# Kernel optimization log

Measured on AMD Instinct MI355X. Metric: run time of the kernel, lower is better.

Reference implementation:

```python
import jax, jax.numpy as jnp
import numpy as np
import math

L, B, T, E, HQ, HKV, V = 6, 4, 1024, 1024, 16, 4, 32000
D = E // HQ          # head dim = 64
G = HQ // HKV        # group size = 4
EKV = E // G         # kv proj dim = 256


def setup_inputs() -> dict:
    key = jax.random.key(0)
    ks = jax.random.split(key, 16)
    def n(k, shape):
        return jax.random.normal(k, shape, jnp.float32) * 0.02
    return dict(
        idx=jax.random.randint(ks[0], (B, T), 0, V),
        wte=n(ks[1], (V, E)),
        Wq=n(ks[2], (L, E, E)), bq=jnp.zeros((L, E), jnp.float32),
        Wk=n(ks[3], (L, EKV, E)), bk=jnp.zeros((L, EKV), jnp.float32),
        Wv=n(ks[4], (L, EKV, E)), bv=jnp.zeros((L, EKV), jnp.float32),
        Wo=n(ks[5], (L, E, E)), bo=jnp.zeros((L, E), jnp.float32),
        ln1_w=jnp.ones((L, E), jnp.float32), ln1_b=jnp.zeros((L, E), jnp.float32),
        ln2_w=jnp.ones((L, E), jnp.float32), ln2_b=jnp.zeros((L, E), jnp.float32),
        Wfc=n(ks[6], (L, 4 * E, E)), bfc=jnp.zeros((L, 4 * E), jnp.float32),
        Wproj=n(ks[7], (L, E, 4 * E)), bproj=jnp.zeros((L, E), jnp.float32),
        lnf_w=jnp.ones((E,), jnp.float32), lnf_b=jnp.zeros((E,), jnp.float32),
        lm_head=n(ks[8], (V, E)),
    )


def _ln(x, w, b):
    m = x.mean(-1, keepdims=True)
    v = ((x - m) ** 2).mean(-1, keepdims=True)
    return (x - m) * jax.lax.rsqrt(v + 1e-5) * w + b


def _gelu_new(x):
    c = math.sqrt(2.0 / math.pi)
    return 0.5 * x * (1.0 + jnp.tanh(c * (x + 0.044715 * x ** 3)))


def _rope_tables(t, d):
    # positions start at 1; thetas = base^(-2*(i-1)/d), i = 1..d/2
    pos = jnp.arange(1, t + 1, dtype=jnp.float32)
    thetas = 10000.0 ** (-2.0 * jnp.arange(d // 2, dtype=jnp.float32) / d)
    ang = pos[:, None] * thetas                      # [t, d/2]
    cos = jnp.concatenate([jnp.cos(ang)] * 2, -1)    # [t, d]
    sin = jnp.concatenate([jnp.sin(ang)] * 2, -1)
    return cos, sin


def _apply_rope(x, cos, sin):
    # x: [b, h, t, d]; x_cos = x; x_sin = concat(-right, left)
    x1, x2 = x[..., : D // 2], x[..., D // 2:]
    return x * cos + jnp.concatenate([-x2, x1], -1) * sin


def _gpt_forward(idx, wte, Wq, bq, Wk, bk, Wv, bv, Wo, bo,
                 ln1_w, ln1_b, ln2_w, ln2_b, Wfc, bfc, Wproj, bproj,
                 lnf_w, lnf_b, lm_head):
    cos, sin = _rope_tables(T, D)
    mask = jnp.tril(jnp.ones((T, T), bool))          # causal
    scale = 1.0 / math.sqrt(D)
    x = wte[idx]                                     # [B, T, E]
    for l in range(L):
        h = _ln(x, ln1_w[l], ln1_b[l])
        q = (h @ Wq[l].T + bq[l]).reshape(B, T, HQ, D).transpose(0, 2, 1, 3)
        k = (h @ Wk[l].T + bk[l]).reshape(B, T, HKV, D).transpose(0, 2, 1, 3)
        v = (h @ Wv[l].T + bv[l]).reshape(B, T, HKV, D).transpose(0, 2, 1, 3)
        q = _apply_rope(q, cos, sin)
        k = _apply_rope(k, cos, sin)
        q = q.reshape(B, HKV, G, T, D)               # kv-major head grouping
        att = jnp.einsum('bhgqd,bhkd->bhgqk', q, k) * scale
        att = jnp.where(mask, att, -jnp.inf)
        att = jax.nn.softmax(att, axis=-1)
        y = jnp.einsum('bhgqk,bhkd->bhgqd', att, v)
        y = y.transpose(0, 3, 1, 2, 4).reshape(B, T, E)   # b q (h g d)
        x = x + (y @ Wo[l].T + bo[l])
        h2 = _ln(x, ln2_w[l], ln2_b[l])
        ff = _gelu_new(h2 @ Wfc[l].T + bfc[l]) @ Wproj[l].T + bproj[l]
        x = x + ff
    x = _ln(x, lnf_w, lnf_b)
    return x @ lm_head.T                             # [B, T, V] logits


def reference(idx, wte, Wq, bq, Wk, bk, Wv, bv, Wo, bo,
              ln1_w, ln1_b, ln2_w, ln2_b, Wfc, bfc, Wproj, bproj,
              lnf_w, lnf_b, lm_head):
    return _gpt_forward(idx, wte, Wq, bq, Wk, bk, Wv, bv, Wo, bo,
                        ln1_w, ln1_b, ln2_w, ln2_b, Wfc, bfc, Wproj, bproj,
                        lnf_w, lnf_b, lm_head)
```

## Files before the change

### kernel.cpp

```cpp
#include <hip/hip_runtime.h>

#define Lz 6
#define Bz 4
#define Tz 1024
#define Ez 1024
#define HQz 16
#define HKVz 4
#define Dz 64
#define EKVz 256
#define Vz 32000
#define FFz 4096
#define QKVz 1536

typedef __attribute__((ext_vector_type(4))) float f32x4;
typedef __attribute__((ext_vector_type(8))) short short8;
typedef unsigned short ushort_t;

__device__ inline ushort_t f2b(float f) {
  union { float f; unsigned u; } x; x.f = f;
  unsigned r = x.u + 0x7fffu + ((x.u >> 16) & 1u);
  return (ushort_t)(r >> 16);
}
__device__ inline float b2f(ushort_t u) {
  union { unsigned u; float f; } x; x.u = ((unsigned)u) << 16;
  return x.f;
}
__device__ inline unsigned packbf(float lo, float hi) {
  return (unsigned)f2b(lo) | ((unsigned)f2b(hi) << 16);
}

__device__ inline void gload16(const void* g, void* l) {
  __builtin_amdgcn_global_load_lds(
      (const __attribute__((address_space(1))) void*)g,
      (__attribute__((address_space(3))) void*)l, 16, 0, 0);
}

template<int BIAS, int GELU, int WF32>
__global__ __launch_bounds__(512, 2) void gemm_bt256(
    const ushort_t* __restrict__ A, const ushort_t* __restrict__ Bw,
    const float* __restrict__ bias,
    float* __restrict__ Cf, ushort_t* __restrict__ Cb,
    int M, int N, int K)
{
  __shared__ ushort_t sA[2][2][128 * 64];
  __shared__ ushort_t sB[2][2][128 * 64];
  const int tid = threadIdx.x;
  const int lane = tid & 63, wid = tid >> 6;
  const int wr = wid >> 2, wc = wid & 3;
  const int l15 = lane & 15, l4 = lane >> 4;

  const int gx = gridDim.x;
  const int nwg = gx * gridDim.y;
  const int orig = blockIdx.y * gx + blockIdx.x;
  const int qq = nwg >> 3, rr = nwg & 7;
  const int xcd = orig & 7, loc = orig >> 3;
  const int swz = (xcd < rr) ? (xcd * (qq + 1) + loc)
                             : (rr * (qq + 1) + (xcd - rr) * qq + loc);
  const int bm = swz % gx, bn = swz / gx;

  const int NT = K >> 6;

  auto stage = [&](const ushort_t* src, int row_base, int k0, ushort_t* dst) {
#pragma unroll
    for (int i = 0; i < 2; ++i) {
      int s = i * 512 + tid;
      int row = s >> 3, jp = s & 7;
      int jlog = jp ^ (row & 7);
      gload16(src + (size_t)(row_base + row) * K + k0 + jlog * 8, (char*)dst + s * 16);
    }
  };

  stage(A,  bm * 256,       0, &sA[0][0][0]);
  stage(A,  bm * 256 + 128, 0, &sA[0][1][0]);
  stage(Bw, bn * 256,       0, &sB[0][0][0]);
  stage(Bw, bn * 256 + 128, 0, &sB[0][1][0]);
  stage(A,  bm * 256,       64, &sA[1][0][0]);
  stage(A,  bm * 256 + 128, 64, &sA[1][1][0]);
  stage(Bw, bn * 256,       64, &sB[1][0][0]);
  stage(Bw, bn * 256 + 128, 64, &sB[1][1][0]);
  asm volatile("s_waitcnt vmcnt(8)" ::: "memory");
  __builtin_amdgcn_sched_barrier(0);
  __builtin_amdgcn_s_barrier();
  __builtin_amdgcn_sched_barrier(0);

  f32x4 acc[8][4] = {};
  const int axc = l15 & 7;

  for (int t = 0; t < NT; ++t) {
    const int b = t & 1;
    const ushort_t* pA = &sA[b][wr][0];
    const ushort_t* pB = &sB[b][wc >> 1][(wc & 1) * 64 * 64];
    short8 aF[8][2], bF[4][2];

#pragma unroll
    for (int mt = 0; mt < 4; ++mt)
#pragma unroll
      for (int ks = 0; ks < 2; ++ks)
        aF[mt][ks] = *(const short8*)&pA[(mt * 16 + l15) * 64 + (((ks << 2) + l4) ^ axc) * 8];
#pragma unroll
    for (int nt = 0; nt < 4; ++nt)
      bF[nt][0] = *(const short8*)&pB[(nt * 16 + l15) * 64 + (l4 ^ axc) * 8];
    __builtin_amdgcn_s_setprio(1);
#pragma unroll
    for (int mt = 0; mt < 4; ++mt)
#pragma unroll
      for (int nt = 0; nt < 4; ++nt)
        acc[mt][nt] = __builtin_amdgcn_mfma_f32_16x16x32_bf16(aF[mt][0], bF[nt][0], acc[mt][nt], 0, 0, 0);
    __builtin_amdgcn_s_setprio(0);

#pragma unroll
    for (int mt = 4; mt < 8; ++mt)
#pragma unroll
      for (int ks = 0; ks < 2; ++ks)
        aF[mt][ks] = *(const short8*)&pA[(mt * 16 + l15) * 64 + (((ks << 2) + l4) ^ axc) * 8];
#pragma unroll
    for (int nt = 0; nt < 4; ++nt)
      bF[nt][1] = *(const short8*)&pB[(nt * 16 + l15) * 64 + ((4 + l4) ^ axc) * 8];
    __builtin_amdgcn_s_setprio(1);
#pragma unroll
    for (int mt = 0; mt < 4; ++mt)
#pragma unroll
      for (int nt = 0; nt < 4; ++nt)
        acc[mt][nt] = __builtin_amdgcn_mfma_f32_16x16x32_bf16(aF[mt][1], bF[nt][1], acc[mt][nt], 0, 0, 0);
    __builtin_amdgcn_s_setprio(0);

    asm volatile("s_waitcnt lgkmcnt(0)" ::: "memory");
    __builtin_amdgcn_sched_barrier(0);
    __builtin_amdgcn_s_barrier();
    __builtin_amdgcn_sched_barrier(0);

    const bool pf = (t + 2 < NT);
    if (pf) {
      const int k2 = (t + 2) << 6;
      stage(Bw, bn * 256,       k2, &sB[b][0][0]);
      stage(Bw, bn * 256 + 128, k2, &sB[b][1][0]);
    }
    __builtin_amdgcn_s_setprio(1);
#pragma unroll
    for (int mt = 4; mt < 8; ++mt)
#pragma unroll
      for (int nt = 0; nt < 4; ++nt)
        acc[mt][nt] = __builtin_amdgcn_mfma_f32_16x16x32_bf16(aF[mt][0], bF[nt][0], acc[mt][nt], 0, 0, 0);
    __builtin_amdgcn_s_setprio(0);

    if (pf) {
      const int k2 = (t + 2) << 6;
      stage(A, bm * 256,       k2, &sA[b][0][0]);
      stage(A, bm * 256 + 128, k2, &sA[b][1][0]);
    }
    __builtin_amdgcn_s_setprio(1);
#pragma unroll
    for (int mt = 4; mt < 8; ++mt)
#pragma unroll
      for (int nt = 0; nt < 4; ++nt)
        acc[mt][nt] = __builtin_amdgcn_mfma_f32_16x16x32_bf16(aF[mt][1], bF[nt][1], acc[mt][nt], 0, 0, 0);
    __builtin_amdgcn_s_setprio(0);

    if (t + 1 < NT) {
      if (pf) { asm volatile("s_waitcnt vmcnt(8)" ::: "memory"); }
      else    { asm volatile("s_waitcnt vmcnt(0)" ::: "memory"); }
      __builtin_amdgcn_sched_barrier(0);
      __builtin_amdgcn_s_barrier();
      __builtin_amdgcn_sched_barrier(0);
    }
  }

#pragma unroll
  for (int mt = 0; mt < 8; ++mt) {
#pragma unroll
    for (int nt = 0; nt < 4; ++nt) {
      const int col = bn * 256 + wc * 64 + nt * 16 + l15;
#pragma unroll
      for (int i = 0; i < 4; ++i) {
        const int row = bm * 256 + wr * 128 + mt * 16 + l4 * 4 + i;
        float v = acc[mt][nt][i];
        if (BIAS) v += bias[col];
        if (GELU) {
          float x = v;
          v = 0.5f * x * (1.f + tanhf(0.7978845608028654f * (x + 0.044715f * x * x * x)));
        }
        const size_t o = (size_t)row * N + col;
        if (WF32) Cf[o] = v; else Cb[o] = f2b(v);
      }
    }
  }
}

template<int BIAS, int RES, int GELU, int WF32, int WBF16, int ROPE>
__global__ __launch_bounds__(256) void gemm_bt(
    const ushort_t* __restrict__ A, const ushort_t* __restrict__ Bw,
    const float* __restrict__ bias, const float* __restrict__ res,
    float* __restrict__ Cf, ushort_t* __restrict__ Cb,
    const float2* __restrict__ tab,
    int M, int N, int K)
{
  __shared__ ushort_t sA[2][128 * 32];
  __shared__ ushort_t sB[2][128 * 32];
  const int tid = threadIdx.x;
  const int lane = tid & 63, wid = tid >> 6;
  const int wm = wid >> 1, wn = wid & 1;
  const int l15 = lane & 15, l4 = lane >> 4;

  const int gx = gridDim.x;
  const int nwg = gx * gridDim.y;
  const int orig = blockIdx.y * gx + blockIdx.x;
  const int qq = nwg >> 3, rr = nwg & 7;
  const int xcd = orig & 7, loc = orig >> 3;
  const int swz = (xcd < rr) ? (xcd * (qq + 1) + loc)
                             : (rr * (qq + 1) + (xcd - rr) * qq + loc);
  const int bm = swz % gx, bn = swz / gx;

  f32x4 acc[4][4] = {};
  const int nK = K >> 5;

#pragma unroll
  for (int j = 0; j < 2; ++j) {
    int s = wid * 128 + j * 64 + lane;
    int row = s >> 2, c8 = (s & 3) << 3;
    gload16(A + (size_t)(bm * 128 + row) * K + c8, (char*)&sA[0][0] + s * 16);
    gload16(Bw + (size_t)(bn * 128 + row) * K + c8, (char*)&sB[0][0] + s * 16);
  }
  __syncthreads();

  int cur = 0;
  for (int kt = 0; kt < nK; ++kt) {
    if (kt + 1 < nK) {
      const int k0 = (kt + 1) << 5;
      const int nb = cur ^ 1;
#pragma unroll
      for (int j = 0; j < 2; ++j) {
        int s = wid * 128 + j * 64 + lane;
        int row = s >> 2, c8 = (s & 3) << 3;
        gload16(A + (size_t)(bm * 128 + row) * K + k0 + c8, (char*)&sA[nb][0] + s * 16);
        gload16(Bw + (size_t)(bn * 128 + row) * K + k0 + c8, (char*)&sB[nb][0] + s * 16);
      }
    }
    short8 aF[4], bF[4];
#pragma unroll
    for (int mt = 0; mt < 4; ++mt)
      aF[mt] = *(const short8*)&sA[cur][(wm * 64 + mt * 16 + l15) * 32 + l4 * 8];
#pragma unroll
    for (int nt = 0; nt < 4; ++nt)
      bF[nt] = *(const short8*)&sB[cur][(wn * 64 + nt * 16 + l15) * 32 + l4 * 8];
#pragma unroll
    for (int mt = 0; mt < 4; ++mt)
#pragma unroll
      for (int nt = 0; nt < 4; ++nt)
        acc[mt][nt] = __builtin_amdgcn_mfma_f32_16x16x32_bf16(aF[mt], bF[nt], acc[mt][nt], 0, 0, 0);
    __syncthreads();
    cur ^= 1;
  }

  if (ROPE) {
    const int col0 = bn * 128 + wn * 64;
    const bool isv = (col0 >= 1280);
#pragma unroll
    for (int mt = 0; mt < 4; ++mt) {
#pragma unroll
      for (int i = 0; i < 4; ++i) {
        const int row = bm * 128 + wm * 64 + mt * 16 + l4 * 4 + i;
        const int t = row & (Tz - 1);
        if (isv) {
#pragma unroll
          for (int nt = 0; nt < 4; ++nt) {
            const int col = col0 + nt * 16 + l15;
            Cb[(size_t)row * N + col] = f2b(acc[mt][nt][i] + bias[col]);
          }
        } else {
#pragma unroll
          for (int nt = 0; nt < 2; ++nt) {
            const int col = col0 + nt * 16 + l15;
            const int jj = nt * 16 + l15;
            const float2 cs = tab[t * 32 + jj];
            const float x1 = acc[mt][nt][i] + bias[col];
            const float x2 = acc[mt][nt + 2][i] + bias[col + 32];
            Cb[(size_t)row * N + col]      = f2b(x1 * cs.x - x2 * cs.y);
            Cb[(size_t)row * N + col + 32] = f2b(x2 * cs.x + x1 * cs.y);
          }
        }
      }
    }
    return;
  }

#pragma unroll
  for (int mt = 0; mt < 4; ++mt) {
#pragma unroll
    for (int nt = 0; nt < 4; ++nt) {
      const int col = bn * 128 + wn * 64 + nt * 16 + l15;
#pragma unroll
      for (int i = 0; i < 4; ++i) {
        const int row = bm * 128 + wm * 64 + mt * 16 + l4 * 4 + i;
        float v = acc[mt][nt][i];
        if (BIAS) v += bias[col];
        if (GELU) {
          float t = v;
          v = 0.5f * t * (1.f + tanhf(0.7978845608028654f * (t + 0.044715f * t * t * t)));
        }
        const size_t o = (size_t)row * N + col;
        if (RES) v += res[o];
        if (WF32) Cf[o] = v;
        if (WBF16) Cb[o] = f2b(v);
      }
    }
  }
}

__global__ __launch_bounds__(256, 4) void attn_k(
    const ushort_t* __restrict__ qkv, const ushort_t* __restrict__ vt,
    ushort_t* __restrict__ y)
{
  __shared__ ushort_t sK[2][64 * 64];
  __shared__ ushort_t sV[2][64 * 64];
  __shared__ unsigned sPu[4][512];
  const int bh = blockIdx.y;
  const int b = bh >> 4, h = bh & 15, hk = h >> 2;
  const int tid = threadIdx.x, lane = tid & 63, wid = tid >> 6;
  const int l15 = lane & 15, l4 = lane >> 4;
  const int xr = l15 & 7;

  for (int pass = 0; pass < 2; ++pass) {
    const int qt = pass ? (int)blockIdx.x : (Tz / 64 - 1 - (int)blockIdx.x);
    const int qrow0 = qt * 64 + wid * 16;
    const int qg = qrow0 + l15;
    const int ntile = qt + 1;

    short8 aQ[2];
#pragma unroll
    for (int ks = 0; ks < 2; ++ks)
      aQ[ks] = *(const short8*)&qkv[(size_t)(b * Tz + qrow0 + l15) * QKVz + h * 64 + ks * 32 + l4 * 8];

    float m = -1e30f, lsum = 0.f;
    f32x4 o[4] = {};

    if (pass) __syncthreads();

#pragma unroll
    for (int j = 0; j < 2; ++j) {
      int s = wid * 128 + j * 64 + lane;
      int row = s >> 3, jp = s & 7, jlog = jp ^ (row & 7);
      gload16(qkv + (size_t)(b * Tz + row) * QKVz + Ez + hk * 64 + jlog * 8, (char*)&sK[0][0] + s * 16);
      gload16(vt + (size_t)((b * HKVz + hk) * 64 + row) * Tz + jlog * 8, (char*)&sV[0][0] + s * 16);
    }

    for (int t = 0; t < ntile; ++t) {
      asm volatile("s_waitcnt vmcnt(0)" ::: "memory");
      __syncthreads();
      if (t + 1 < ntile) {
        const int nb = (t + 1) & 1;
#pragma unroll
        for (int j = 0; j < 2; ++j) {
          int s = wid * 128 + j * 64 + lane;
          int row = s >> 3, jp = s & 7, jlog = jp ^ (row & 7);
          gload16(qkv + (size_t)(b * Tz + (t + 1) * 64 + row) * QKVz + Ez + hk * 64 + jlog * 8,
                  (char*)&sK[nb][0] + s * 16);
          gload16(vt + (size_t)((b * HKVz + hk) * 64 + row) * Tz + (t + 1) * 64 + jlog * 8,
                  (char*)&sV[nb][0] + s * 16);
        }
      }
      const ushort_t* K = &sK[t & 1][0];
      const ushort_t* V = &sV[t & 1][0];

      f32x4 sacc[4] = {};
#pragma unroll
      for (int nt = 0; nt < 4; ++nt) {
#pragma unroll
        for (int ks = 0; ks < 2; ++ks) {
          short8 aK = *(const short8*)&K[(nt * 16 + l15) * 64 + (((ks << 2) + l4) ^ xr) * 8];
          sacc[nt] = __builtin_amdgcn_mfma_f32_16x16x32_bf16(aK, aQ[ks], sacc[nt], 0, 0, 0);
        }
      }

      float sv[4][4];
      float pmax = -1e30f;
#pragma unroll
      for (int nt = 0; nt < 4; ++nt)
#pragma unroll
        for (int i = 0; i < 4; ++i) {
          int key = t * 64 + nt * 16 + l4 * 4 + i;
          float s = sacc[nt][i] * 0.125f;
          if (key > qg) s = -1e30f;
          sv[nt][i] = s;
          pmax = fmaxf(pmax, s);
        }
      pmax = fmaxf(pmax, __shfl_xor(pmax, 16));
      pmax = fmaxf(pmax, __shfl_xor(pmax, 32));
      const float mnew = fmaxf(m, pmax);
      const float corr = __expf(m - mnew);
      float psum = 0.f;
#pragma unroll
      for (int nt = 0; nt < 4; ++nt)
#pragma unroll
        for (int i = 0; i < 4; ++i) {
          float p = __expf(sv[nt][i] - mnew);
          sv[nt][i] = p;
          psum += p;
        }
      psum += __shfl_xor(psum, 16);
      psum += __shfl_xor(psum, 32);
      lsum = lsum * corr + psum;
      m = mnew;
#pragma unroll
      for (int dt = 0; dt < 4; ++dt) o[dt] *= corr;

#pragma unroll
      for (int nt = 0; nt < 4; ++nt) {
        uint2 u;
        u.x = packbf(sv[nt][0], sv[nt][1]);
        u.y = packbf(sv[nt][2], sv[nt][3]);
        *(uint2*)&sPu[wid][l15 * 32 + (((nt * 2 + (l4 >> 1)) ^ xr) << 2) + ((l4 & 1) << 1)] = u;
      }
      short8 aP[2];
#pragma unroll
      for (int ks = 0; ks < 2; ++ks)
        aP[ks] = *(const short8*)&sPu[wid][l15 * 32 + ((((ks << 2) + l4) ^ xr) << 2)];

#pragma unroll
      for (int dt = 0; dt < 4; ++dt) {
#pragma unroll
        for (int ks = 0; ks < 2; ++ks) {
          short8 aV = *(const short8*)&V[(dt * 16 + l15) * 64 + (((ks << 2) + l4) ^ xr) * 8];
          o[dt] = __builtin_amdgcn_mfma_f32_16x16x32_bf16(aV, aP[ks], o[dt], 0, 0, 0);
        }
      }
    }

    const float inv = 1.f / lsum;
    const size_t yrow = (size_t)(b * Tz + qrow0 + l15) * Ez + h * 64;
#pragma unroll
    for (int dt = 0; dt < 4; ++dt) {
      ushort4 w;
      w.x = f2b(o[dt][0] * inv);
      w.y = f2b(o[dt][1] * inv);
      w.z = f2b(o[dt][2] * inv);
      w.w = f2b(o[dt][3] * inv);
      *(ushort4*)&y[yrow + dt * 16 + l4 * 4] = w;
    }
  }
}

__global__ __launch_bounds__(256) void vtrans_k(
    const ushort_t* __restrict__ qkv, ushort_t* __restrict__ vt)
{
  __shared__ ushort_t tile[64][72];
  const int tt = blockIdx.x, bh = blockIdx.y;
  const int b = bh >> 2, hk = bh & 3;
  const int tid = threadIdx.x;
  {
    const int r = tid >> 2, c0 = (tid & 3) * 16;
    const ushort_t* src = qkv + (size_t)(b * Tz + tt * 64 + r) * QKVz + 1280 + hk * 64 + c0;
    *(short8*)&tile[r][c0] = *(const short8*)src;
    *(short8*)&tile[r][c0 + 8] = *(const short8*)(src + 8);
  }
  __syncthreads();
  {
    const int d = tid >> 2, t0 = (tid & 3) * 16;
    ushort_t* dst = vt + (size_t)((b * HKVz + hk) * 64 + d) * Tz + tt * 64 + t0;
    short8 o0, o1;
#pragma unroll
    for (int ii = 0; ii < 8; ++ii) { o0[ii] = (short)tile[t0 + ii][d]; o1[ii] = (short)tile[t0 + 8 + ii][d]; }
    *(short8*)dst = o0;
    *(short8*)(dst + 8) = o1;
  }
}

__global__ __launch_bounds__(256) void ln_bf16(
    const float* __restrict__ x, const float* __restrict__ w,
    const float* __restrict__ b, ushort_t* __restrict__ out)
{
  __shared__ float red[8];
  const int row = blockIdx.x, tid = threadIdx.x;
  float4 vv = *(const float4*)&x[(size_t)row * Ez + tid * 4];
  float s = vv.x + vv.y + vv.z + vv.w;
  float sq = vv.x * vv.x + vv.y * vv.y + vv.z * vv.z + vv.w * vv.w;
#pragma unroll
  for (int off = 1; off < 64; off <<= 1) { s += __shfl_xor(s, off); sq += __shfl_xor(sq, off); }
  if ((tid & 63) == 0) { red[(tid >> 6) * 2] = s; red[(tid >> 6) * 2 + 1] = sq; }
  __syncthreads();
  const float ts = red[0] + red[2] + red[4] + red[6];
  const float tq = red[1] + red[3] + red[5] + red[7];
  const float mean = ts * (1.f / Ez);
  const float var = tq * (1.f / Ez) - mean * mean;
  const float rstd = rsqrtf(var + 1e-5f);
  float4 wv = *(const float4*)&w[tid * 4];
  float4 bv = *(const float4*)&b[tid * 4];
  ushort4 ov;
  ov.x = f2b((vv.x - mean) * rstd * wv.x + bv.x);
  ov.y = f2b((vv.y - mean) * rstd * wv.y + bv.y);
  ov.z = f2b((vv.z - mean) * rstd * wv.z + bv.z);
  ov.w = f2b((vv.w - mean) * rstd * wv.w + bv.w);
  *(ushort4*)&out[(size_t)row * Ez + tid * 4] = ov;
}

__global__ __launch_bounds__(256) void embed_k(
    const int* __restrict__ idx, const float* __restrict__ wte, float* __restrict__ x)
{
  int i = blockIdx.x * 256 + threadIdx.x;
  int row = i >> 8, c = (i & 255) << 2;
  *(float4*)&x[(size_t)row * Ez + c] = *(const float4*)&wte[(size_t)idx[row] * Ez + c];
}

__global__ __launch_bounds__(256) void cvt_bf16(
    const float* __restrict__ in, ushort_t* __restrict__ out, int n)
{
  int i = (blockIdx.x * 256 + threadIdx.x) * 4;
  if (i >= n) return;
  float4 v = *(const float4*)&in[i];
  ushort4 o;
  o.x = f2b(v.x); o.y = f2b(v.y); o.z = f2b(v.z); o.w = f2b(v.w);
  *(ushort4*)&out[i] = o;
}

__global__ __launch_bounds__(256) void cvt_layer(
    const float* __restrict__ Wq, const float* __restrict__ Wk,
    const float* __restrict__ Wv, const float* __restrict__ Wo_,
    const float* __restrict__ Wfc_, const float* __restrict__ Wpj_,
    ushort_t* __restrict__ wqkv, ushort_t* __restrict__ wo,
    ushort_t* __restrict__ wfc, ushort_t* __restrict__ wpj)
{
  int i = (blockIdx.x * 256 + threadIdx.x) * 4;
  const float* src; ushort_t* dst; int off;
  if (i < 1048576)       { src = Wq;   dst = wqkv;           off = i; }
  else if (i < 1310720)  { src = Wk;   dst = wqkv + 1048576; off = i - 1048576; }
  else if (i < 1572864)  { src = Wv;   dst = wqkv + 1310720; off = i - 1310720; }
  else if (i < 2621440)  { src = Wo_;  dst = wo;             off = i - 1572864; }
  else if (i < 6815744)  { src = Wfc_; dst = wfc;            off = i - 2621440; }
  else                   { src = Wpj_; dst = wpj;            off = i - 6815744; }
  float4 v = *(const float4*)&src[off];
  ushort4 o;
  o.x = f2b(v.x); o.y = f2b(v.y); o.z = f2b(v.z); o.w = f2b(v.w);
  *(ushort4*)&dst[off] = o;
}

__global__ __launch_bounds__(256) void rope_tab_k(float2* __restrict__ tab)
{
  int i = blockIdx.x * 256 + threadIdx.x;
  int t = i >> 5, j = i & 31;
  float theta = powf(10000.0f, -(float)j / 32.0f);
  float ang = (float)(t + 1) * theta;
  tab[i] = make_float2(cosf(ang), sinf(ang));
}

__global__ __launch_bounds__(256) void biascat_all(
    const float* __restrict__ bq, const float* __restrict__ bk,
    const float* __restrict__ bv, float* __restrict__ out)
{
  int i = blockIdx.x * 256 + threadIdx.x;
  int l = i / QKVz, j = i - l * QKVz;
  float v = (j < Ez) ? bq[l * Ez + j]
          : ((j < Ez + EKVz) ? bk[l * EKVz + j - Ez] : bv[l * EKVz + j - Ez - EKVz]);
  out[i] = v;
}

template<int BIAS, int RES, int GELU, int WF32, int WBF16, int ROPE = 0>
static void launch_gemm(const ushort_t* A, const ushort_t* Bw, const float* bias,
                        const float* res, float* Cf, ushort_t* Cb, const float* tab,
                        int M, int N, int K, hipStream_t s)
{
  dim3 g(M / 128, N / 128);
  gemm_bt<BIAS, RES, GELU, WF32, WBF16, ROPE><<<g, 256, 0, s>>>(
      A, Bw, bias, res, Cf, Cb, (const float2*)tab, M, N, K);
}

extern "C" void kernel_launch(void* const* d_in, const int* in_sizes, int n_in,
                              void* d_out, int out_size, void* d_ws, size_t ws_size,
                              hipStream_t stream)
{
  (void)in_sizes; (void)n_in; (void)out_size; (void)ws_size;
  const int*   idx   = (const int*)d_in[0];
  const float* wte   = (const float*)d_in[1];
  const float* Wq    = (const float*)d_in[2];
  const float* bq    = (const float*)d_in[3];
  const float* Wk    = (const float*)d_in[4];
  const float* bk    = (const float*)d_in[5];
  const float* Wv    = (const float*)d_in[6];
  const float* bv    = (const float*)d_in[7];
  const float* Wo    = (const float*)d_in[8];
  const float* bo    = (const float*)d_in[9];
  const float* ln1w  = (const float*)d_in[10];
  const float* ln1b  = (const float*)d_in[11];
  const float* ln2w  = (const float*)d_in[12];
  const float* ln2b  = (const float*)d_in[13];
  const float* Wfc   = (const float*)d_in[14];
  const float* bfc   = (const float*)d_in[15];
  const float* Wproj = (const float*)d_in[16];
  const float* bproj = (const float*)d_in[17];
  const float* lnfw  = (const float*)d_in[18];
  const float* lnfb  = (const float*)d_in[19];
  const float* lmh   = (const float*)d_in[20];
  float* out = (float*)d_out;

  char* ws = (char*)d_ws;
  size_t off = 0;
  auto alloc = [&](size_t bytes) -> void* {
    void* p = ws + off;
    off += (bytes + 255) & ~(size_t)255;
    return p;
  };
  ushort_t* wbuf  = (ushort_t*)alloc((size_t)Vz * Ez * 2);
  float*    x     = (float*)alloc((size_t)Bz * Tz * Ez * 4);
  ushort_t* hb    = (ushort_t*)alloc((size_t)Bz * Tz * Ez * 2);
  ushort_t* qkvb  = (ushort_t*)alloc((size_t)Bz * Tz * QKVz * 2);
  ushort_t* vtb   = (ushort_t*)alloc((size_t)Bz * HKVz * 64 * Tz * 2);
  ushort_t* yb    = (ushort_t*)alloc((size_t)Bz * Tz * Ez * 2);
  ushort_t* ffb   = (ushort_t*)alloc((size_t)Bz * Tz * FFz * 2);
  float*    tab   = (float*)alloc((size_t)Tz * 32 * 2 * 4);
  float*    qbia  = (float*)alloc((size_t)Lz * QKVz * 4);

  ushort_t* wqkv = wbuf;
  ushort_t* wo   = wqkv + (size_t)QKVz * Ez;
  ushort_t* wfc  = wo + (size_t)Ez * Ez;
  ushort_t* wpj  = wfc + (size_t)FFz * Ez;

  const int M = Bz * Tz;

  rope_tab_k<<<Tz * 32 / 256, 256, 0, stream>>>((float2*)tab);
  biascat_all<<<Lz * QKVz / 256, 256, 0, stream>>>(bq, bk, bv, qbia);
  embed_k<<<Bz * Tz, 256, 0, stream>>>(idx, wte, x);

  for (int l = 0; l < Lz; ++l) {
    ln_bf16<<<M, 256, 0, stream>>>(x, ln1w + l * Ez, ln1b + l * Ez, hb);
    cvt_layer<<<10752, 256, 0, stream>>>(
        Wq + (size_t)l * Ez * Ez, Wk + (size_t)l * EKVz * Ez, Wv + (size_t)l * EKVz * Ez,
        Wo + (size_t)l * Ez * Ez, Wfc + (size_t)l * FFz * Ez, Wproj + (size_t)l * Ez * FFz,
        wqkv, wo, wfc, wpj);
    launch_gemm<1, 0, 0, 0, 1, 1>(hb, wqkv, qbia + l * QKVz, nullptr, nullptr, qkvb, tab,
                                  M, QKVz, Ez, stream);
    vtrans_k<<<dim3(Tz / 64, Bz * HKVz), 256, 0, stream>>>(qkvb, vtb);
    attn_k<<<dim3(Tz / 128, Bz * HQz), 256, 0, stream>>>(qkvb, vtb, yb);
    launch_gemm<1, 1, 0, 1, 0>(yb, wo, bo + l * Ez, x, x, nullptr, nullptr, M, Ez, Ez, stream);
    ln_bf16<<<M, 256, 0, stream>>>(x, ln2w + l * Ez, ln2b + l * Ez, hb);
    {
      dim3 g(M / 256, FFz / 256);
      gemm_bt256<1, 1, 0><<<g, 512, 0, stream>>>(hb, wfc, bfc + l * FFz, nullptr, ffb, M, FFz, Ez);
    }
    launch_gemm<1, 1, 0, 1, 0>(ffb, wpj, bproj + l * Ez, x, x, nullptr, nullptr, M, Ez, FFz, stream);
  }
  ln_bf16<<<M, 256, 0, stream>>>(x, lnfw, lnfb, hb);
  cvt_bf16<<<(Vz * Ez / 4 + 255) / 256, 256, 0, stream>>>(lmh, wbuf, Vz * Ez);
  {
    dim3 g(M / 256, Vz / 256);
    gemm_bt256<0, 0, 1><<<g, 512, 0, stream>>>(hb, wbuf, nullptr, out, nullptr, M, Vz, Ez);
  }
}
```

Before: 1.881 ms.

## Store residual stream in bf16 and fuse V transpose into QKV GEMM epilogue

The residual stream x changes from fp32 to bf16 storage. The embedding, layernorm and residual-add GEMM epilogues now read and write bf16, which halves residual memory traffic. The separate vtrans kernel is removed: the QKV GEMM epilogue writes V directly in transposed [b,hk,d,t] layout using 4-element vector stores, saving one launch and one read/write pass. The cost is lower precision in the residual accumulation across layers, which may hurt accuracy, and strided scattered stores for the V tile.

```diff
diff --git a/kernel.cpp b/kernel.cpp
--- a/kernel.cpp
+++ b/kernel.cpp
@@ -189,9 +189,9 @@
 template<int BIAS, int RES, int GELU, int WF32, int WBF16, int ROPE>
 __global__ __launch_bounds__(256) void gemm_bt(
     const ushort_t* __restrict__ A, const ushort_t* __restrict__ Bw,
-    const float* __restrict__ bias, const float* __restrict__ res,
+    const float* __restrict__ bias, const ushort_t* __restrict__ res,
     float* __restrict__ Cf, ushort_t* __restrict__ Cb,
-    const float2* __restrict__ tab,
+    ushort_t* __restrict__ vtb, const float2* __restrict__ tab,
     int M, int N, int K)
 {
   __shared__ ushort_t sA[2][128 * 32];
@@ -256,17 +256,25 @@
     const bool isv = (col0 >= 1280);
 #pragma unroll
     for (int mt = 0; mt < 4; ++mt) {
-#pragma unroll
-      for (int i = 0; i < 4; ++i) {
-        const int row = bm * 128 + wm * 64 + mt * 16 + l4 * 4 + i;
-        const int t = row & (Tz - 1);
-        if (isv) {
-#pragma unroll
-          for (int nt = 0; nt < 4; ++nt) {
-            const int col = col0 + nt * 16 + l15;
-            Cb[(size_t)row * N + col] = f2b(acc[mt][nt][i] + bias[col]);
-          }
-        } else {
+      const int row_base = bm * 128 + wm * 64 + mt * 16 + l4 * 4;
+      const int bb = row_base >> 10, t0 = row_base & (Tz - 1);
+      if (isv) {
+#pragma unroll
+        for (int nt = 0; nt < 4; ++nt) {
+          const int col = col0 + nt * 16 + l15;
+          const int cm = col - 1280, hk = cm >> 6, d = cm & 63;
+          ushort4 w;
+          w.x = f2b(acc[mt][nt][0] + bias[col]);
+          w.y = f2b(acc[mt][nt][1] + bias[col]);
+          w.z = f2b(acc[mt][nt][2] + bias[col]);
+          w.w = f2b(acc[mt][nt][3] + bias[col]);
+          *(ushort4*)&vtb[((size_t)(bb * HKVz + hk) * 64 + d) * Tz + t0] = w;
+        }
+      } else {
+#pragma unroll
+        for (int i = 0; i < 4; ++i) {
+          const int row = row_base + i;
+          const int t = row & (Tz - 1);
 #pragma unroll
           for (int nt = 0; nt < 2; ++nt) {
             const int col = col0 + nt * 16 + l15;
@@ -298,7 +306,7 @@
           v = 0.5f * t * (1.f + tanhf(0.7978845608028654f * (t + 0.044715f * t * t * t)));
         }
         const size_t o = (size_t)row * N + col;
-        if (RES) v += res[o];
+        if (RES) v += b2f(res[o]);
         if (WF32) Cf[o] = v;
         if (WBF16) Cb[o] = f2b(v);
       }
@@ -439,40 +447,16 @@
   }
 }
 
-__global__ __launch_bounds__(256) void vtrans_k(
-    const ushort_t* __restrict__ qkv, ushort_t* __restrict__ vt)
-{
-  __shared__ ushort_t tile[64][72];
-  const int tt = blockIdx.x, bh = blockIdx.y;
-  const int b = bh >> 2, hk = bh & 3;
-  const int tid = threadIdx.x;
-  {
-    const int r = tid >> 2, c0 = (tid & 3) * 16;
-    const ushort_t* src = qkv + (size_t)(b * Tz + tt * 64 + r) * QKVz + 1280 + hk * 64 + c0;
-    *(short8*)&tile[r][c0] = *(const short8*)src;
-    *(short8*)&tile[r][c0 + 8] = *(const short8*)(src + 8);
-  }
-  __syncthreads();
-  {
-    const int d = tid >> 2, t0 = (tid & 3) * 16;
-    ushort_t* dst = vt + (size_t)((b * HKVz + hk) * 64 + d) * Tz + tt * 64 + t0;
-    short8 o0, o1;
-#pragma unroll
-    for (int ii = 0; ii < 8; ++ii) { o0[ii] = (short)tile[t0 + ii][d]; o1[ii] = (short)tile[t0 + 8 + ii][d]; }
-    *(short8*)dst = o0;
-    *(short8*)(dst + 8) = o1;
-  }
-}
-
 __global__ __launch_bounds__(256) void ln_bf16(
-    const float* __restrict__ x, const float* __restrict__ w,
+    const ushort_t* __restrict__ x, const float* __restrict__ w,
     const float* __restrict__ b, ushort_t* __restrict__ out)
 {
   __shared__ float red[8];
   const int row = blockIdx.x, tid = threadIdx.x;
-  float4 vv = *(const float4*)&x[(size_t)row * Ez + tid * 4];
-  float s = vv.x + vv.y + vv.z + vv.w;
-  float sq = vv.x * vv.x + vv.y * vv.y + vv.z * vv.z + vv.w * vv.w;
+  ushort4 xv = *(const ushort4*)&x[(size_t)row * Ez + tid * 4];
+  float v0 = b2f(xv.x), v1 = b2f(xv.y), v2 = b2f(xv.z), v3 = b2f(xv.w);
+  float s = v0 + v1 + v2 + v3;
+  float sq = v0 * v0 + v1 * v1 + v2 * v2 + v3 * v3;
 #pragma unroll
   for (int off = 1; off < 64; off <<= 1) { s += __shfl_xor(s, off); sq += __shfl_xor(sq, off); }
   if ((tid & 63) == 0) { red[(tid >> 6) * 2] = s; red[(tid >> 6) * 2 + 1] = sq; }
@@ -485,19 +469,22 @@
   float4 wv = *(const float4*)&w[tid * 4];
   float4 bv = *(const float4*)&b[tid * 4];
   ushort4 ov;
-  ov.x = f2b((vv.x - mean) * rstd * wv.x + bv.x);
-  ov.y = f2b((vv.y - mean) * rstd * wv.y + bv.y);
-  ov.z = f2b((vv.z - mean) * rstd * wv.z + bv.z);
-  ov.w = f2b((vv.w - mean) * rstd * wv.w + bv.w);
+  ov.x = f2b((v0 - mean) * rstd * wv.x + bv.x);
+  ov.y = f2b((v1 - mean) * rstd * wv.y + bv.y);
+  ov.z = f2b((v2 - mean) * rstd * wv.z + bv.z);
+  ov.w = f2b((v3 - mean) * rstd * wv.w + bv.w);
   *(ushort4*)&out[(size_t)row * Ez + tid * 4] = ov;
 }
 
 __global__ __launch_bounds__(256) void embed_k(
-    const int* __restrict__ idx, const float* __restrict__ wte, float* __restrict__ x)
+    const int* __restrict__ idx, const float* __restrict__ wte, ushort_t* __restrict__ x)
 {
   int i = blockIdx.x * 256 + threadIdx.x;
   int row = i >> 8, c = (i & 255) << 2;
-  *(float4*)&x[(size_t)row * Ez + c] = *(const float4*)&wte[(size_t)idx[row] * Ez + c];
+  float4 v = *(const float4*)&wte[(size_t)idx[row] * Ez + c];
+  ushort4 o;
+  o.x = f2b(v.x); o.y = f2b(v.y); o.z = f2b(v.z); o.w = f2b(v.w);
+  *(ushort4*)&x[(size_t)row * Ez + c] = o;
 }
 
 __global__ __launch_bounds__(256) void cvt_bf16(
@@ -554,12 +541,13 @@
 
 template<int BIAS, int RES, int GELU, int WF32, int WBF16, int ROPE = 0>
 static void launch_gemm(const ushort_t* A, const ushort_t* Bw, const float* bias,
-                        const float* res, float* Cf, ushort_t* Cb, const float* tab,
+                        const ushort_t* res, float* Cf, ushort_t* Cb,
+                        ushort_t* vtb, const float* tab,
                         int M, int N, int K, hipStream_t s)
 {
   dim3 g(M / 128, N / 128);
   gemm_bt<BIAS, RES, GELU, WF32, WBF16, ROPE><<<g, 256, 0, s>>>(
-      A, Bw, bias, res, Cf, Cb, (const float2*)tab, M, N, K);
+      A, Bw, bias, res, Cf, Cb, vtb, (const float2*)tab, M, N, K);
 }
 
 extern "C" void kernel_launch(void* const* d_in, const int* in_sizes, int n_in,
@@ -598,7 +586,7 @@
     return p;
   };
   ushort_t* wbuf  = (ushort_t*)alloc((size_t)Vz * Ez * 2);
-  float*    x     = (float*)alloc((size_t)Bz * Tz * Ez * 4);
+  ushort_t* x     = (ushort_t*)alloc((size_t)Bz * Tz * Ez * 2);
   ushort_t* hb    = (ushort_t*)alloc((size_t)Bz * Tz * Ez * 2);
   ushort_t* qkvb  = (ushort_t*)alloc((size_t)Bz * Tz * QKVz * 2);
   ushort_t* vtb   = (ushort_t*)alloc((size_t)Bz * HKVz * 64 * Tz * 2);
@@ -624,17 +612,16 @@
         Wq + (size_t)l * Ez * Ez, Wk + (size_t)l * EKVz * Ez, Wv + (size_t)l * EKVz * Ez,
         Wo + (size_t)l * Ez * Ez, Wfc + (size_t)l * FFz * Ez, Wproj + (size_t)l * Ez * FFz,
         wqkv, wo, wfc, wpj);
-    launch_gemm<1, 0, 0, 0, 1, 1>(hb, wqkv, qbia + l * QKVz, nullptr, nullptr, qkvb, tab,
+    launch_gemm<1, 0, 0, 0, 1, 1>(hb, wqkv, qbia + l * QKVz, nullptr, nullptr, qkvb, vtb, tab,
                                   M, QKVz, Ez, stream);
-    vtrans_k<<<dim3(Tz / 64, Bz * HKVz), 256, 0, stream>>>(qkvb, vtb);
     attn_k<<<dim3(Tz / 128, Bz * HQz), 256, 0, stream>>>(qkvb, vtb, yb);
-    launch_gemm<1, 1, 0, 1, 0>(yb, wo, bo + l * Ez, x, x, nullptr, nullptr, M, Ez, Ez, stream);
+    launch_gemm<1, 1, 0, 0, 1>(yb, wo, bo + l * Ez, x, nullptr, x, nullptr, nullptr, M, Ez, Ez, stream);
     ln_bf16<<<M, 256, 0, stream>>>(x, ln2w + l * Ez, ln2b + l * Ez, hb);
     {
       dim3 g(M / 256, FFz / 256);
       gemm_bt256<1, 1, 0><<<g, 512, 0, stream>>>(hb, wfc, bfc + l * FFz, nullptr, ffb, M, FFz, Ez);
     }
-    launch_gemm<1, 1, 0, 1, 0>(ffb, wpj, bproj + l * Ez, x, x, nullptr, nullptr, M, Ez, FFz, stream);
+    launch_gemm<1, 1, 0, 0, 1>(ffb, wpj, bproj + l * Ez, x, nullptr, x, nullptr, nullptr, M, Ez, FFz, stream);
   }
   ln_bf16<<<M, 256, 0, stream>>>(x, lnfw, lnfb, hb);
   cvt_bf16<<<(Vz * Ez / 4 + 255) / 256, 256, 0, stream>>>(lmh, wbuf, Vz * Ez);
```

Measured after the change: 1.829 ms. -2.8%, faster.
